# Performance work log

Measured on AMD Instinct MI355X. Metric: run time of the kernel, lower is better.

The kernel has to match this reference:

```python
import jax, jax.numpy as jnp
import numpy as np

N, DEG, D, D2, B, NEG = 65536, 16, 64, 128, 1024, 10
EPS = 1e-12  # F.normalize eps


def setup_inputs() -> dict:
    key = jax.random.key(0)
    ks = jax.random.split(key, 9)
    s1 = 1.0 / np.sqrt(2 * D)
    s2 = 1.0 / np.sqrt(2 * D)
    return {
        "feat_data": jax.random.normal(ks[0], (N, D), jnp.float32),
        "adj": jax.random.randint(ks[1], (N, DEG), 0, N),
        "inputs1": jax.random.randint(ks[2], (B,), 0, N),
        "inputs2": jax.random.randint(ks[3], (B,), 0, N),
        "neg": jax.random.randint(ks[4], (NEG,), 0, N),
        "W1": jax.random.uniform(ks[5], (D, 2 * D), jnp.float32, -s1, s1),
        "b1": jax.random.uniform(ks[6], (D,), jnp.float32, -s1, s1),
        "W2": jax.random.uniform(ks[7], (D2, 2 * D), jnp.float32, -s2, s2),
        "b2": jax.random.uniform(ks[8], (D2,), jnp.float32, -s2, s2),
    }


def reference(feat_data, adj, inputs1, inputs2, neg, W1, b1, W2, b2):
    # Hop-1: per-node neighbor feature sum (gather + reduce), concat self, linear1, tanh.
    # Computed for all nodes (superset of the union the original builds; same values).
    sum1 = feat_data[adj].sum(axis=1)                      # [N, D] gather-heavy
    h1 = jnp.tanh(jnp.concatenate([feat_data, sum1], axis=-1) @ W1.T + b1)  # [N, D]

    def emb(nodes):
        # Hop-2: sum hop-1 embeddings of neighbors, concat raw self features, linear2.
        sum2 = h1[adj[nodes]].sum(axis=1)                  # [b, D]
        out = jnp.concatenate([feat_data[nodes], sum2], axis=-1) @ W2.T + b2  # [b, D2]
        nrm = jnp.maximum(jnp.linalg.norm(out, axis=1, keepdims=True), EPS)
        return out / nrm

    return emb(inputs1), emb(inputs2), emb(neg)
```

## Files before the change

### kernel.cpp

```cpp
#include <hip/hip_runtime.h>
#include <math.h>

#define NN   65536
#define DEGC 16
#define DD   64
#define DD2  128
#define BB   1024
#define NEGC 10
#define NROWS (2 * BB + NEGC)
#define NEDGE (NROWS * DEGC)

__device__ __forceinline__ float tanh_fast(float x) {
    float t = __expf(2.0f * x);
    return 1.0f - 2.0f * __builtin_amdgcn_rcpf(t + 1.0f);
}

__global__ __launch_bounds__(256) void hop1_fused(
    const float* __restrict__ feat, const int* __restrict__ adj,
    const int* __restrict__ in1, const int* __restrict__ in2,
    const int* __restrict__ neg,
    const float* __restrict__ W1, const float* __restrict__ b1,
    float* __restrict__ buf) {

    __shared__ float wt[DD2 * 65];

    int tid = threadIdx.x;
    #pragma unroll
    for (int t = 0; t < (DD * DD2) / 256; ++t) {
        int lin = t * 256 + tid;
        int j = lin >> 7, i = lin & 127;
        wt[i * 65 + j] = W1[lin];
    }

    int lane = tid & 63;
    int w = tid >> 6;
    int r = blockIdx.x;
    int node = (r < BB) ? in1[r] : (r < 2 * BB ? in2[r - BB] : neg[r - 2 * BB]);
    node = __builtin_amdgcn_readfirstlane(node);

    int n[4];
    #pragma unroll
    for (int m = 0; m < 4; ++m)
        n[m] = __builtin_amdgcn_readfirstlane(adj[node * DEGC + w * 4 + m]);

    int ebase = r * DEGC + w * 4;

    #pragma unroll
    for (int m = 0; m < 4; ++m) {
        const int* arow = adj + n[m] * DEGC;
        float g[DEGC];
        #pragma unroll
        for (int k2 = 0; k2 < DEGC; ++k2)
            g[k2] = feat[arow[k2] * DD + lane];
        float p0 = (g[0] + g[1]) + (g[2] + g[3]);
        float p1 = (g[4] + g[5]) + (g[6] + g[7]);
        float p2 = (g[8] + g[9]) + (g[10] + g[11]);
        float p3 = (g[12] + g[13]) + (g[14] + g[15]);
        buf[(size_t)(ebase + m) * DD + lane] = (p0 + p1) + (p2 + p3);
    }

    __syncthreads();

    float bias = b1[lane];
    float a0 = bias, a1 = bias, a2 = bias, a3 = bias;

    const float* f0 = feat + (size_t)n[0] * DD;
    const float* f1 = feat + (size_t)n[1] * DD;
    const float* f2 = feat + (size_t)n[2] * DD;
    const float* f3 = feat + (size_t)n[3] * DD;

    #pragma unroll
    for (int i4 = 0; i4 < 16; ++i4) {
        float w0 = wt[(i4 * 4 + 0) * 65 + lane];
        float w1v = wt[(i4 * 4 + 1) * 65 + lane];
        float w2v = wt[(i4 * 4 + 2) * 65 + lane];
        float w3v = wt[(i4 * 4 + 3) * 65 + lane];
        float4 c0 = *(const float4*)(f0 + i4 * 4);
        float4 c1 = *(const float4*)(f1 + i4 * 4);
        float4 c2 = *(const float4*)(f2 + i4 * 4);
        float4 c3 = *(const float4*)(f3 + i4 * 4);
        a0 += c0.x * w0 + c0.y * w1v + c0.z * w2v + c0.w * w3v;
        a1 += c1.x * w0 + c1.y * w1v + c1.z * w2v + c1.w * w3v;
        a2 += c2.x * w0 + c2.y * w1v + c2.z * w2v + c2.w * w3v;
        a3 += c3.x * w0 + c3.y * w1v + c3.z * w2v + c3.w * w3v;
    }
    const float* s0 = buf + (size_t)(ebase + 0) * DD;
    const float* s1 = buf + (size_t)(ebase + 1) * DD;
    const float* s2 = buf + (size_t)(ebase + 2) * DD;
    const float* s3 = buf + (size_t)(ebase + 3) * DD;
    #pragma unroll
    for (int i4 = 0; i4 < 16; ++i4) {
        float w0 = wt[(DD + i4 * 4 + 0) * 65 + lane];
        float w1v = wt[(DD + i4 * 4 + 1) * 65 + lane];
        float w2v = wt[(DD + i4 * 4 + 2) * 65 + lane];
        float w3v = wt[(DD + i4 * 4 + 3) * 65 + lane];
        float4 c0 = *(const float4*)(s0 + i4 * 4);
        float4 c1 = *(const float4*)(s1 + i4 * 4);
        float4 c2 = *(const float4*)(s2 + i4 * 4);
        float4 c3 = *(const float4*)(s3 + i4 * 4);
        a0 += c0.x * w0 + c0.y * w1v + c0.z * w2v + c0.w * w3v;
        a1 += c1.x * w0 + c1.y * w1v + c1.z * w2v + c1.w * w3v;
        a2 += c2.x * w0 + c2.y * w1v + c2.z * w2v + c2.w * w3v;
        a3 += c3.x * w0 + c3.y * w1v + c3.z * w2v + c3.w * w3v;
    }

    buf[(size_t)(ebase + 0) * DD + lane] = tanh_fast(a0);
    buf[(size_t)(ebase + 1) * DD + lane] = tanh_fast(a1);
    buf[(size_t)(ebase + 2) * DD + lane] = tanh_fast(a2);
    buf[(size_t)(ebase + 3) * DD + lane] = tanh_fast(a3);
}

__global__ __launch_bounds__(256) void hop2_fused(
    const float* __restrict__ feat, const float* __restrict__ h1,
    const int* __restrict__ in1, const int* __restrict__ in2,
    const int* __restrict__ neg,
    const float* __restrict__ W2, const float* __restrict__ b2,
    float* __restrict__ out) {

    __shared__ float4 q2[4096];
    __shared__ float4 cs4[8][16];

    int tid = threadIdx.x;
    {
        int j = tid & 127, g0 = tid >> 7;
        #pragma unroll
        for (int g = 0; g < 16; ++g) {
            int i4 = g0 * 16 + g;
            q2[(i4 << 7) | j] = *(const float4*)(W2 + j * DD2 + (i4 << 2));
        }
    }

    int lane = tid & 63;
    int w = tid >> 6;
    int r0 = blockIdx.x * 8 + w * 2;
    int r1 = r0 + 1;
    bool a0 = r0 < NROWS, a1 = r1 < NROWS;

    #pragma unroll
    for (int m = 0; m < 2; ++m) {
        int r = r0 + m;
        if (r < NROWS) {
            const float* base = h1 + (size_t)r * DEGC * DD;
            float s = 0.f;
            #pragma unroll
            for (int k = 0; k < DEGC; ++k)
                s += base[k * DD + lane];
            ((float*)&cs4[w * 2 + m][0])[lane] = s;
        }
    }
    __syncthreads();

    int node0 = a0 ? ((r0 < BB) ? in1[r0] : (r0 < 2 * BB ? in2[r0 - BB] : neg[r0 - 2 * BB])) : 0;
    int node1 = a1 ? ((r1 < BB) ? in1[r1] : (r1 < 2 * BB ? in2[r1 - BB] : neg[r1 - 2 * BB])) : node0;
    node0 = __builtin_amdgcn_readfirstlane(node0);
    node1 = __builtin_amdgcn_readfirstlane(node1);
    const float* cf0 = feat + node0 * DD;
    const float* cf1 = feat + node1 * DD;

    float A0 = b2[lane], B0 = b2[DD + lane];
    float A1 = A0, B1 = B0;

    #pragma unroll
    for (int i4 = 0; i4 < 16; ++i4) {
        float4 wA = q2[(i4 << 7) | lane];
        float4 wB = q2[(i4 << 7) | (64 + lane)];
        float4 c0 = *(const float4*)(cf0 + (i4 << 2));
        float4 c1 = *(const float4*)(cf1 + (i4 << 2));
        A0 += c0.x * wA.x + c0.y * wA.y + c0.z * wA.z + c0.w * wA.w;
        B0 += c0.x * wB.x + c0.y * wB.y + c0.z * wB.z + c0.w * wB.w;
        A1 += c1.x * wA.x + c1.y * wA.y + c1.z * wA.z + c1.w * wA.w;
        B1 += c1.x * wB.x + c1.y * wB.y + c1.z * wB.z + c1.w * wB.w;
    }
    #pragma unroll
    for (int i4 = 0; i4 < 16; ++i4) {
        float4 wA = q2[((16 + i4) << 7) | lane];
        float4 wB = q2[((16 + i4) << 7) | (64 + lane)];
        float4 c0 = cs4[w * 2 + 0][i4];
        float4 c1 = cs4[w * 2 + 1][i4];
        A0 += c0.x * wA.x + c0.y * wA.y + c0.z * wA.z + c0.w * wA.w;
        B0 += c0.x * wB.x + c0.y * wB.y + c0.z * wB.z + c0.w * wB.w;
        A1 += c1.x * wA.x + c1.y * wA.y + c1.z * wA.z + c1.w * wA.w;
        B1 += c1.x * wB.x + c1.y * wB.y + c1.z * wB.z + c1.w * wB.w;
    }

    if (a0) {
        float ss = A0 * A0 + B0 * B0;
        #pragma unroll
        for (int off = 32; off > 0; off >>= 1) ss += __shfl_xor(ss, off, 64);
        float inv = 1.0f / fmaxf(sqrtf(ss), 1e-12f);
        out[r0 * DD2 + lane]      = A0 * inv;
        out[r0 * DD2 + DD + lane] = B0 * inv;
    }
    if (a1) {
        float ss = A1 * A1 + B1 * B1;
        #pragma unroll
        for (int off = 32; off > 0; off >>= 1) ss += __shfl_xor(ss, off, 64);
        float inv = 1.0f / fmaxf(sqrtf(ss), 1e-12f);
        out[r1 * DD2 + lane]      = A1 * inv;
        out[r1 * DD2 + DD + lane] = B1 * inv;
    }
}

extern "C" void kernel_launch(void* const* d_in, const int* in_sizes, int n_in,
                              void* d_out, int out_size, void* d_ws, size_t ws_size,
                              hipStream_t stream) {
    const float* feat = (const float*)d_in[0];
    const int*   adj  = (const int*)d_in[1];
    const int*   in1  = (const int*)d_in[2];
    const int*   in2  = (const int*)d_in[3];
    const int*   neg  = (const int*)d_in[4];
    const float* W1   = (const float*)d_in[5];
    const float* b1   = (const float*)d_in[6];
    const float* W2   = (const float*)d_in[7];
    const float* b2   = (const float*)d_in[8];
    float* out = (float*)d_out;

    float* buf = (float*)d_ws;

    hop1_fused<<<NROWS, 256, 0, stream>>>(feat, adj, in1, in2, neg, W1, b1, buf);
    hop2_fused<<<(NROWS + 7) / 8, 256, 0, stream>>>(
        feat, buf, in1, in2, neg, W2, b2, out);
}
```

Measured before the change: 62.25 us.

## Split hop-1 into separate gather and GEMV kernels with float4 weight layout

Hop-1 was one kernel per row, with each wave doing four serial 16-neighbor gathers before a block barrier and the GEMV. It is now split in two. A gather kernel gives one wave per edge and records each neighbor id in workspace. A GEMV kernel then reads those ids and the gathered sums, using W1 staged in shared memory as float4 per lane instead of a padded scalar transpose. The aim is more memory-level parallelism in the gather and fewer LDS reads in the GEMV. In exchange it adds a third kernel launch and a global round trip for the gathered sums and node ids.

Result: slower. 70.02 us (+12.5%).

```diff
diff --git a/kernel.cpp b/kernel.cpp
--- a/kernel.cpp
+++ b/kernel.cpp
@@ -15,93 +15,92 @@
     return 1.0f - 2.0f * __builtin_amdgcn_rcpf(t + 1.0f);
 }
 
-__global__ __launch_bounds__(256) void hop1_fused(
+__global__ __launch_bounds__(256) void gather1_kernel(
     const float* __restrict__ feat, const int* __restrict__ adj,
     const int* __restrict__ in1, const int* __restrict__ in2,
     const int* __restrict__ neg,
-    const float* __restrict__ W1, const float* __restrict__ b1,
+    float* __restrict__ buf, int* __restrict__ nodes_e) {
+
+    int lane = threadIdx.x & 63;
+    int e = blockIdx.x * 4 + (threadIdx.x >> 6);
+    int r = e >> 4, k = e & 15;
+    int node = (r < BB) ? in1[r] : (r < 2 * BB ? in2[r - BB] : neg[r - 2 * BB]);
+    node = __builtin_amdgcn_readfirstlane(node);
+    int n = __builtin_amdgcn_readfirstlane(adj[node * DEGC + k]);
+    const int* arow = adj + n * DEGC;
+    float g[DEGC];
+    #pragma unroll
+    for (int k2 = 0; k2 < DEGC; ++k2)
+        g[k2] = feat[arow[k2] * DD + lane];
+    float p0 = (g[0] + g[1]) + (g[2] + g[3]);
+    float p1 = (g[4] + g[5]) + (g[6] + g[7]);
+    float p2 = (g[8] + g[9]) + (g[10] + g[11]);
+    float p3 = (g[12] + g[13]) + (g[14] + g[15]);
+    buf[(size_t)e * DD + lane] = (p0 + p1) + (p2 + p3);
+    if (lane == 0) nodes_e[e] = n;
+}
+
+__global__ __launch_bounds__(256) void gemv1_kernel(
+    const float* __restrict__ feat, const float* __restrict__ W1,
+    const float* __restrict__ b1, const int* __restrict__ nodes_e,
     float* __restrict__ buf) {
 
-    __shared__ float wt[DD2 * 65];
-
+    __shared__ float4 q[2048];
     int tid = threadIdx.x;
-    #pragma unroll
-    for (int t = 0; t < (DD * DD2) / 256; ++t) {
-        int lin = t * 256 + tid;
-        int j = lin >> 7, i = lin & 127;
-        wt[i * 65 + j] = W1[lin];
-    }
+    {
+        int j = tid & 63, g = tid >> 6;
+        #pragma unroll
+        for (int t = 0; t < 8; ++t) {
+            int i4 = g * 8 + t;
+            q[(i4 << 6) | j] = *(const float4*)(W1 + j * DD2 + i4 * 4);
+        }
+    }
+    __syncthreads();
 
     int lane = tid & 63;
     int w = tid >> 6;
-    int r = blockIdx.x;
-    int node = (r < BB) ? in1[r] : (r < 2 * BB ? in2[r - BB] : neg[r - 2 * BB]);
-    node = __builtin_amdgcn_readfirstlane(node);
-
-    int n[4];
-    #pragma unroll
-    for (int m = 0; m < 4; ++m)
-        n[m] = __builtin_amdgcn_readfirstlane(adj[node * DEGC + w * 4 + m]);
-
-    int ebase = r * DEGC + w * 4;
-
-    #pragma unroll
-    for (int m = 0; m < 4; ++m) {
-        const int* arow = adj + n[m] * DEGC;
-        float g[DEGC];
-        #pragma unroll
-        for (int k2 = 0; k2 < DEGC; ++k2)
-            g[k2] = feat[arow[k2] * DD + lane];
-        float p0 = (g[0] + g[1]) + (g[2] + g[3]);
-        float p1 = (g[4] + g[5]) + (g[6] + g[7]);
-        float p2 = (g[8] + g[9]) + (g[10] + g[11]);
-        float p3 = (g[12] + g[13]) + (g[14] + g[15]);
-        buf[(size_t)(ebase + m) * DD + lane] = (p0 + p1) + (p2 + p3);
-    }
-
-    __syncthreads();
+    int ebase = blockIdx.x * DEGC + w * 4;
+
+    int n0 = __builtin_amdgcn_readfirstlane(nodes_e[ebase + 0]);
+    int n1 = __builtin_amdgcn_readfirstlane(nodes_e[ebase + 1]);
+    int n2 = __builtin_amdgcn_readfirstlane(nodes_e[ebase + 2]);
+    int n3 = __builtin_amdgcn_readfirstlane(nodes_e[ebase + 3]);
+
+    const float* f0 = feat + (size_t)n0 * DD;
+    const float* f1 = feat + (size_t)n1 * DD;
+    const float* f2 = feat + (size_t)n2 * DD;
+    const float* f3 = feat + (size_t)n3 * DD;
+    const float* s0 = buf + (size_t)(ebase + 0) * DD;
+    const float* s1 = buf + (size_t)(ebase + 1) * DD;
+    const float* s2 = buf + (size_t)(ebase + 2) * DD;
+    const float* s3 = buf + (size_t)(ebase + 3) * DD;
 
     float bias = b1[lane];
     float a0 = bias, a1 = bias, a2 = bias, a3 = bias;
 
-    const float* f0 = feat + (size_t)n[0] * DD;
-    const float* f1 = feat + (size_t)n[1] * DD;
-    const float* f2 = feat + (size_t)n[2] * DD;
-    const float* f3 = feat + (size_t)n[3] * DD;
-
-    #pragma unroll
-    for (int i4 = 0; i4 < 16; ++i4) {
-        float w0 = wt[(i4 * 4 + 0) * 65 + lane];
-        float w1v = wt[(i4 * 4 + 1) * 65 + lane];
-        float w2v = wt[(i4 * 4 + 2) * 65 + lane];
-        float w3v = wt[(i4 * 4 + 3) * 65 + lane];
+    #pragma unroll
+    for (int i4 = 0; i4 < 16; ++i4) {
+        float4 wv = q[(i4 << 6) | lane];
         float4 c0 = *(const float4*)(f0 + i4 * 4);
         float4 c1 = *(const float4*)(f1 + i4 * 4);
         float4 c2 = *(const float4*)(f2 + i4 * 4);
         float4 c3 = *(const float4*)(f3 + i4 * 4);
-        a0 += c0.x * w0 + c0.y * w1v + c0.z * w2v + c0.w * w3v;
-        a1 += c1.x * w0 + c1.y * w1v + c1.z * w2v + c1.w * w3v;
-        a2 += c2.x * w0 + c2.y * w1v + c2.z * w2v + c2.w * w3v;
-        a3 += c3.x * w0 + c3.y * w1v + c3.z * w2v + c3.w * w3v;
-    }
-    const float* s0 = buf + (size_t)(ebase + 0) * DD;
-    const float* s1 = buf + (size_t)(ebase + 1) * DD;
-    const float* s2 = buf + (size_t)(ebase + 2) * DD;
-    const float* s3 = buf + (size_t)(ebase + 3) * DD;
-    #pragma unroll
-    for (int i4 = 0; i4 < 16; ++i4) {
-        float w0 = wt[(DD + i4 * 4 + 0) * 65 + lane];
-        float w1v = wt[(DD + i4 * 4 + 1) * 65 + lane];
-        float w2v = wt[(DD + i4 * 4 + 2) * 65 + lane];
-        float w3v = wt[(DD + i4 * 4 + 3) * 65 + lane];
+        a0 += c0.x * wv.x + c0.y * wv.y + c0.z * wv.z + c0.w * wv.w;
+        a1 += c1.x * wv.x + c1.y * wv.y + c1.z * wv.z + c1.w * wv.w;
+        a2 += c2.x * wv.x + c2.y * wv.y + c2.z * wv.z + c2.w * wv.w;
+        a3 += c3.x * wv.x + c3.y * wv.y + c3.z * wv.z + c3.w * wv.w;
+    }
+    #pragma unroll
+    for (int i4 = 0; i4 < 16; ++i4) {
+        float4 wv = q[((16 + i4) << 6) | lane];
         float4 c0 = *(const float4*)(s0 + i4 * 4);
         float4 c1 = *(const float4*)(s1 + i4 * 4);
         float4 c2 = *(const float4*)(s2 + i4 * 4);
         float4 c3 = *(const float4*)(s3 + i4 * 4);
-        a0 += c0.x * w0 + c0.y * w1v + c0.z * w2v + c0.w * w3v;
-        a1 += c1.x * w0 + c1.y * w1v + c1.z * w2v + c1.w * w3v;
-        a2 += c2.x * w0 + c2.y * w1v + c2.z * w2v + c2.w * w3v;
-        a3 += c3.x * w0 + c3.y * w1v + c3.z * w2v + c3.w * w3v;
+        a0 += c0.x * wv.x + c0.y * wv.y + c0.z * wv.z + c0.w * wv.w;
+        a1 += c1.x * wv.x + c1.y * wv.y + c1.z * wv.z + c1.w * wv.w;
+        a2 += c2.x * wv.x + c2.y * wv.y + c2.z * wv.z + c2.w * wv.w;
+        a3 += c3.x * wv.x + c3.y * wv.y + c3.z * wv.z + c3.w * wv.w;
     }
 
     buf[(size_t)(ebase + 0) * DD + lane] = tanh_fast(a0);
@@ -215,9 +214,12 @@
     const float* b2   = (const float*)d_in[8];
     float* out = (float*)d_out;
 
-    float* buf = (float*)d_ws;
-
-    hop1_fused<<<NROWS, 256, 0, stream>>>(feat, adj, in1, in2, neg, W1, b1, buf);
+    float* buf     = (float*)d_ws;
+    int*   nodes_e = (int*)((char*)d_ws + (size_t)NEDGE * DD * sizeof(float));
+
+    gather1_kernel<<<NEDGE / 4, 256, 0, stream>>>(
+        feat, adj, in1, in2, neg, buf, nodes_e);
+    gemv1_kernel<<<NROWS, 256, 0, stream>>>(feat, W1, b1, nodes_e, buf);
     hop2_fused<<<(NROWS + 7) / 8, 256, 0, stream>>>(
         feat, buf, in1, in2, neg, W2, b2, out);
 }
```
